# Optimization experiments

Hardware: AMD Instinct MI355X
Metric: run time of the kernel (lower is better)

The kernel has to match this reference:

```python
import jax, jax.numpy as jnp
import numpy as np

NH, NL, NPNT = 8, 4, 4          # heads, levels, points
NQ, BS, NK, D, DFFN = 100, 8, 18, 256, 1024
SPATIAL = np.array([[92, 92], [46, 46], [23, 23], [12, 12]], np.int32)
LEN_MEM = int((SPATIAL[:, 0] * SPATIAL[:, 1]).sum())  # 11253


def _layernorm(x, g, b):
    m = x.mean(-1, keepdims=True)
    v = ((x - m) ** 2).mean(-1, keepdims=True)
    return (x - m) / jnp.sqrt(v + 1e-5) * g + b


def _mha(xq, xk, xv, in_w, in_b, out_w, out_b):
    # torch nn.MultiheadAttention semantics, inputs (S, B, D)
    S, B, d = xq.shape
    dh = d // NH
    wq, wk, wv = jnp.split(in_w, 3, axis=0)
    bq, bk, bv = jnp.split(in_b, 3, axis=0)
    def proj(x, w, b):
        return (x @ w.T + b).reshape(x.shape[0], B, NH, dh).transpose(1, 2, 0, 3)
    q = proj(xq, wq, bq) * (1.0 / np.sqrt(dh))
    k = proj(xk, wk, bk)
    v = proj(xv, wv, bv)
    att = jax.nn.softmax(jnp.einsum('bhqd,bhkd->bhqk', q, k), axis=-1)
    o = jnp.einsum('bhqk,bhkd->bhqd', att, v).transpose(2, 0, 1, 3).reshape(S, B, d)
    return o @ out_w.T + out_b


def _bilinear(v_l, loc):
    # v_l: (bs,H,W,NH,dh); loc: (bs,Lq,NH,P,2) normalized [0,1]
    # matches F.grid_sample(align_corners=False, padding_mode='zeros')
    bs, H, W, nh, dh = v_l.shape
    x = loc[..., 0] * W - 0.5
    y = loc[..., 1] * H - 0.5
    x0 = jnp.floor(x); y0 = jnp.floor(y)
    lx = x - x0; ly = y - y0
    b_idx = jnp.arange(bs)[:, None, None, None]
    h_idx = jnp.arange(nh)[None, None, :, None]
    def corner(xa, ya, w):
        valid = (xa >= 0) & (xa < W) & (ya >= 0) & (ya < H)
        xi = jnp.clip(xa, 0, W - 1).astype(jnp.int32)
        yi = jnp.clip(ya, 0, H - 1).astype(jnp.int32)
        return v_l[b_idx, yi, xi, h_idx] * (w * valid)[..., None]
    return (corner(x0, y0, (1 - lx) * (1 - ly)) + corner(x0 + 1, y0, lx * (1 - ly))
            + corner(x0, y0 + 1, (1 - lx) * ly) + corner(x0 + 1, y0 + 1, lx * ly))


def _msda(q, rp, mem, pad_mask, ss, off_w, off_b, aw_w, aw_b, val_w, val_b, outp_w, outp_b):
    bs, Lq, d = q.shape
    dh = d // NH
    value = mem @ val_w.T + val_b
    value = jnp.where(pad_mask[..., None], 0.0, value).reshape(bs, -1, NH, dh)
    off = (q @ off_w.T + off_b).reshape(bs, Lq, NH, NL, NPNT, 2)
    aw = jax.nn.softmax((q @ aw_w.T + aw_b).reshape(bs, Lq, NH, NL * NPNT), -1)
    aw = aw.reshape(bs, Lq, NH, NL, NPNT)
    wh = jnp.asarray(ss[:, ::-1].copy(), jnp.float32)  # offset normalizer (W, H)
    loc = rp[:, :, None, :, None, :] + off / wh[None, None, None, :, None, :]
    out = jnp.zeros((bs, Lq, NH, dh), q.dtype)
    start = 0
    for l in range(NL):
        H, W = int(ss[l, 0]), int(ss[l, 1])
        v_l = value[:, start:start + H * W].reshape(bs, H, W, NH, dh)
        start += H * W
        samp = _bilinear(v_l, loc[:, :, :, l])          # (bs,Lq,NH,P,dh)
        out = out + (samp * aw[:, :, :, l, :, None]).sum(3)
    return out.reshape(bs, Lq, d) @ outp_w.T + outp_b


def _forward(tgt_pose, pos, ref_points, memory, w_in_w, w_in_b, w_out_w, w_out_b,
             a_in_w, a_in_b, a_out_w, a_out_b, off_w, off_b, aw_w, aw_b,
             val_w, val_b, outp_w, outp_b, wn_g, wn_b, an_g, an_b,
             n1_g, n1_b, n2_g, n2_b, l1_w, l1_b, l2_w, l2_b,
             spatial_shapes, level_start_index, padding_mask):
    ss = np.asarray(jax.device_get(spatial_shapes))
    nq, bs, nk, d = tgt_pose.shape
    # within-group self-attn over the nk keypoint tokens.
    # NOTE: with_pos_embed mutates tgt_pose in place in the torch code, so
    # q = k = v = tgt + pos and the residual also uses tgt + pos (faithful).
    t = tgt_pose + pos
    x = t.reshape(nq * bs, nk, d).transpose(1, 0, 2)   # (nk, nq*bs, d)
    a1 = _mha(x, x, x, w_in_w, w_in_b, w_out_w, w_out_b)
    t = _layernorm(t + a1.transpose(1, 0, 2).reshape(nq, bs, nk, d), wn_g, wn_b)
    # across-group self-attn over the nq groups
    x2 = t.reshape(nq, bs * nk, d)
    a2 = _mha(x2, x2, x2, a_in_w, a_in_b, a_out_w, a_out_b)
    t = _layernorm(t + a2.reshape(nq, bs, nk, d), an_g, an_b)
    # MSDeformAttn cross-attention (in-place pos add again, faithful)
    t = t + pos
    q = t.transpose(1, 0, 2, 3).reshape(bs, nq * nk, d)
    rp = jnp.swapaxes(ref_points, 0, 1)                # (bs, nq*nk, NL, 2)
    mem = jnp.swapaxes(memory, 0, 1)                   # (bs, LEN_MEM, d)
    c = _msda(q, rp, mem, padding_mask, ss, off_w, off_b, aw_w, aw_b,
              val_w, val_b, outp_w, outp_b)
    c = c.reshape(bs, nq, nk, d).transpose(1, 0, 2, 3)
    t = _layernorm(t + c, n1_g, n1_b)
    # FFN (dropout is identity in eval)
    h = jax.nn.relu(t @ l1_w.T + l1_b)
    return _layernorm(t + (h @ l2_w.T + l2_b), n2_g, n2_b)


def setup_inputs() -> dict:
    key = jax.random.key(0)
    ks = jax.random.split(key, 16)
    p = lambda k, shape: jax.random.normal(k, shape, jnp.float32) * 0.02
    lsi = np.concatenate([[0], np.cumsum(SPATIAL[:, 0] * SPATIAL[:, 1])[:-1]]).astype(np.int32)
    return {
        'tgt_pose': jax.random.normal(ks[0], (NQ, BS, NK, D), jnp.float32),
        'pos': jax.random.normal(ks[1], (NQ, BS, NK, D), jnp.float32),
        'ref_points': jax.random.uniform(ks[2], (NQ * NK, BS, NL, 2), jnp.float32),
        'memory': jax.random.normal(ks[3], (LEN_MEM, BS, D), jnp.float32),
        'w_in_w': p(ks[4], (3 * D, D)), 'w_in_b': jnp.zeros((3 * D,)),
        'w_out_w': p(ks[5], (D, D)), 'w_out_b': jnp.zeros((D,)),
        'a_in_w': p(ks[6], (3 * D, D)), 'a_in_b': jnp.zeros((3 * D,)),
        'a_out_w': p(ks[7], (D, D)), 'a_out_b': jnp.zeros((D,)),
        'off_w': p(ks[8], (NH * NL * NPNT * 2, D)),
        'off_b': jax.random.uniform(ks[9], (NH * NL * NPNT * 2,), jnp.float32, -2.0, 2.0),
        'aw_w': p(ks[10], (NH * NL * NPNT, D)), 'aw_b': jnp.zeros((NH * NL * NPNT,)),
        'val_w': p(ks[11], (D, D)), 'val_b': jnp.zeros((D,)),
        'outp_w': p(ks[12], (D, D)), 'outp_b': jnp.zeros((D,)),
        'wn_g': jnp.ones((D,)), 'wn_b': jnp.zeros((D,)),
        'an_g': jnp.ones((D,)), 'an_b': jnp.zeros((D,)),
        'n1_g': jnp.ones((D,)), 'n1_b': jnp.zeros((D,)),
        'n2_g': jnp.ones((D,)), 'n2_b': jnp.zeros((D,)),
        'l1_w': p(ks[13], (DFFN, D)), 'l1_b': jnp.zeros((DFFN,)),
        'l2_w': p(ks[14], (D, DFFN)), 'l2_b': jnp.zeros((D,)),
        'spatial_shapes': jnp.asarray(SPATIAL),
        'level_start_index': jnp.asarray(lsi),
        'padding_mask': jnp.zeros((BS, LEN_MEM), bool),
    }


def reference(tgt_pose, pos, ref_points, memory, w_in_w, w_in_b, w_out_w, w_out_b,
              a_in_w, a_in_b, a_out_w, a_out_b, off_w, off_b, aw_w, aw_b,
              val_w, val_b, outp_w, outp_b, wn_g, wn_b, an_g, an_b,
              n1_g, n1_b, n2_g, n2_b, l1_w, l1_b, l2_w, l2_b,
              spatial_shapes, level_start_index, padding_mask):
    return _forward(tgt_pose, pos, ref_points, memory, w_in_w, w_in_b, w_out_w, w_out_b,
                    a_in_w, a_in_b, a_out_w, a_out_b, off_w, off_b, aw_w, aw_b,
                    val_w, val_b, outp_w, outp_b, wn_g, wn_b, an_g, an_b,
                    n1_g, n1_b, n2_g, n2_b, l1_w, l1_b, l2_w, l2_b,
                    spatial_shapes, level_start_index, padding_mask)
```

## Files before the change

### kernel.cpp

```cpp
#include <hip/hip_runtime.h>
#include <math.h>

#define NH_ 8
#define D_ 256
#define NK_ 18
#define NQ_ 100
#define BS_ 8
#define LQ_ 1800
#define LEN_MEM_ 11253
#define NTOK_ 14400

typedef short bf16x8 __attribute__((ext_vector_type(8)));
typedef float f32x4 __attribute__((ext_vector_type(4)));
typedef unsigned short ushort;

__device__ inline ushort f2bf(float f) {
    unsigned int u = __builtin_bit_cast(unsigned int, f);
    unsigned int r = (u + 0x7fffu + ((u >> 16) & 1u)) >> 16;
    return (ushort)r;
}
__device__ inline float bf2f_hi(unsigned int u) {
    unsigned int i = u & 0xffff0000u;
    return __builtin_bit_cast(float, i);
}
__device__ inline float bf2f_lo(unsigned int u) {
    unsigned int i = u << 16;
    return __builtin_bit_cast(float, i);
}
__device__ inline int packbf2(float a, float b) {
    return (int)f2bf(a) | ((int)f2bf(b) << 16);
}

__global__ __launch_bounds__(256)
void wcvt_kernel(const float* s0, const float* s1, const float* s2, const float* s3,
                 const float* s4, const float* s5, const float* s6, const float* s7,
                 const float* s8, const float* s9, ushort* dst) {
    const int sizes[10] = {196608,65536,196608,65536,65536,32768,65536,65536,262144,262144};
    const int offs[10]  = {0,196608,262144,458752,524288,589824,622592,688128,753664,1015808};
    int ti = blockIdx.y;
    const float* s;
    switch (ti) {
        case 0: s = s0; break; case 1: s = s1; break; case 2: s = s2; break;
        case 3: s = s3; break; case 4: s = s4; break; case 5: s = s5; break;
        case 6: s = s6; break; case 7: s = s7; break; case 8: s = s8; break;
        default: s = s9; break;
    }
    int n = sizes[ti];
    int i = (blockIdx.x * 256 + threadIdx.x) * 8;
    if (i >= n) return;
    ushort* d = dst + offs[ti] + i;
    float4 f0 = *(const float4*)(s + i);
    float4 f1 = *(const float4*)(s + i + 4);
    int4 val;
    val.x = packbf2(f0.x, f0.y);
    val.y = packbf2(f0.z, f0.w);
    val.z = packbf2(f1.x, f1.y);
    val.w = packbf2(f1.z, f1.w);
    *(int4*)d = val;
}

__global__ __launch_bounds__(256)
void addcvt_kernel(const float* __restrict__ a, const float* __restrict__ b,
                   float* __restrict__ c, ushort* __restrict__ cbf, int n4) {
    int i = blockIdx.x * blockDim.x + threadIdx.x;
    if (i >= n4) return;
    float4 av = ((const float4*)a)[i];
    float4 bv = ((const float4*)b)[i];
    float4 cv;
    cv.x = av.x + bv.x; cv.y = av.y + bv.y; cv.z = av.z + bv.z; cv.w = av.w + bv.w;
    ((float4*)c)[i] = cv;
    uint2 p;
    p.x = (unsigned int)packbf2(cv.x, cv.y);
    p.y = (unsigned int)packbf2(cv.z, cv.w);
    *(uint2*)(cbf + (size_t)i * 4) = p;
}

template<int MODE, bool RELU, bool A_F32, bool OUT_BF16, int BN, int WAVES, int R>
__device__ __forceinline__
void gemmw_body(int bx, int by, const void* __restrict__ Av, const ushort* __restrict__ W,
                const float* __restrict__ bias, void* __restrict__ Cv,
                int M, int N, const unsigned char* __restrict__ mask, ushort* Ws) {
    constexpr int K = 256;
    constexpr int NT = BN / 16;
    const int tid = threadIdx.x;
    const int m0 = bx * (WAVES * 16 * R);
    const int n0 = by * BN;

    for (int c = tid; c < 32 * BN; c += WAVES * 64) {
        int kc = c & 31, n = c >> 5;
        int dst = kc * BN + (n ^ (kc & 7));
        *(int4*)(Ws + dst * 8) = *(const int4*)(W + (long)(n0 + n) * K + kc * 8);
    }
    __syncthreads();

    const int wv = tid >> 6, lane = tid & 63, fr = lane & 15, hi = lane >> 4;
    const int wm0 = m0 + wv * (16 * R);
    long arow[R];
#pragma unroll
    for (int r = 0; r < R; ++r) {
        int gr = wm0 + r * 16 + fr;
        if (gr > M - 1) gr = M - 1;
        if (MODE == 2) {
            int b = gr / LQ_; int lq = gr - b * LQ_;
            int q = lq / NK_; int kk = lq - q * NK_;
            arow[r] = (long)q * (BS_ * NK_) + b * NK_ + kk;
        } else {
            arow[r] = gr;
        }
    }

    f32x4 acc[R][NT];
#pragma unroll
    for (int r = 0; r < R; ++r)
#pragma unroll
        for (int t = 0; t < NT; ++t) acc[r][t] = f32x4{0.f, 0.f, 0.f, 0.f};

    if (A_F32) {
        const float* ap[R];
        float4 p0[R], p1[R];
#pragma unroll
        for (int r = 0; r < R; ++r) {
            ap[r] = (const float*)Av + arow[r] * (long)K + hi * 8;
            p0[r] = *(const float4*)ap[r];
            p1[r] = *(const float4*)(ap[r] + 4);
        }
#pragma unroll
        for (int ks = 0; ks < 8; ++ks) {
            bf16x8 cur[R];
#pragma unroll
            for (int r = 0; r < R; ++r) {
                int4 v;
                v.x = packbf2(p0[r].x, p0[r].y); v.y = packbf2(p0[r].z, p0[r].w);
                v.z = packbf2(p1[r].x, p1[r].y); v.w = packbf2(p1[r].z, p1[r].w);
                cur[r] = __builtin_bit_cast(bf16x8, v);
                if (ks < 7) {
                    p0[r] = *(const float4*)(ap[r] + (ks + 1) * 32);
                    p1[r] = *(const float4*)(ap[r] + (ks + 1) * 32 + 4);
                }
            }
            const int kc = ks * 4 + hi;
            const ushort* wb = Ws + ((kc * BN) + (fr ^ (kc & 7))) * 8;
#pragma unroll
            for (int t = 0; t < NT; ++t) {
                bf16x8 wf = *(const bf16x8*)(wb + t * 128);
#pragma unroll
                for (int r = 0; r < R; ++r)
                    acc[r][t] = __builtin_amdgcn_mfma_f32_16x16x32_bf16(cur[r], wf, acc[r][t], 0, 0, 0);
            }
        }
    } else {
        const ushort* ap[R];
        bf16x8 afrag[R];
#pragma unroll
        for (int r = 0; r < R; ++r) {
            ap[r] = (const ushort*)Av + arow[r] * (long)K + hi * 8;
            afrag[r] = *(const bf16x8*)ap[r];
        }
#pragma unroll
        for (int ks = 0; ks < 8; ++ks) {
            bf16x8 cur[R];
#pragma unroll
            for (int r = 0; r < R; ++r) {
                cur[r] = afrag[r];
                if (ks < 7) afrag[r] = *(const bf16x8*)(ap[r] + (ks + 1) * 32);
            }
            const int kc = ks * 4 + hi;
            const ushort* wb = Ws + ((kc * BN) + (fr ^ (kc & 7))) * 8;
#pragma unroll
            for (int t = 0; t < NT; ++t) {
                bf16x8 wf = *(const bf16x8*)(wb + t * 128);
#pragma unroll
                for (int r = 0; r < R; ++r)
                    acc[r][t] = __builtin_amdgcn_mfma_f32_16x16x32_bf16(cur[r], wf, acc[r][t], 0, 0, 0);
            }
        }
    }

#pragma unroll
    for (int r = 0; r < R; ++r) {
#pragma unroll
        for (int rr = 0; rr < 4; ++rr) {
            int gm = wm0 + r * 16 + hi * 4 + rr;
            if (gm >= M) continue;
            long orow = gm;
            bool zero = false;
            if (MODE == 1) {
                if (mask && mask[(size_t)(gm & 7) * LEN_MEM_ + (gm >> 3)]) zero = true;
            } else if (MODE == 3) {
                int b = gm / LQ_; int lq = gm - b * LQ_;
                int q = lq / NK_; int kk = lq - q * NK_;
                orow = (long)q * (BS_ * NK_) + b * NK_ + kk;
            }
#pragma unroll
            for (int t = 0; t < NT; ++t) {
                int gn = n0 + t * 16 + fr;
                float v = acc[r][t][rr] + bias[gn];
                if (RELU) v = fmaxf(v, 0.f);
                if (zero) v = 0.f;
                if (OUT_BF16) ((ushort*)Cv)[orow * (long)N + gn] = f2bf(v);
                else ((float*)Cv)[orow * (long)N + gn] = v;
            }
        }
    }
}

template<int MODE, bool RELU, bool A_F32, bool OUT_BF16, int BN, int WAVES, int R>
__global__ __launch_bounds__(WAVES * 64)
void gemmw_kernel(const void* __restrict__ Av, const ushort* __restrict__ W,
                  const float* __restrict__ bias, void* __restrict__ Cv,
                  int M, int N, const unsigned char* __restrict__ mask) {
    __shared__ ushort Ws[32 * BN * 8];
    gemmw_body<MODE, RELU, A_F32, OUT_BF16, BN, WAVES, R>(
        blockIdx.x, blockIdx.y, Av, W, bias, Cv, M, N, mask, Ws);
}

__global__ __launch_bounds__(512)
void fusedqv_kernel(const float* __restrict__ memA, const ushort* __restrict__ Wv,
                    const float* __restrict__ bv, ushort* __restrict__ Cval,
                    const unsigned char* __restrict__ mask, int voff,
                    const ushort* __restrict__ Aq, const ushort* __restrict__ Wq,
                    const float* __restrict__ bq, ushort* __restrict__ Cq) {
    __shared__ ushort Ws[32 * 128 * 8];
    int idx = blockIdx.x;
    if ((idx & 1) == 0) {
        int v = voff + (idx >> 1);
        gemmw_body<1, false, true, true, 128, 8, 2>(v >> 1, v & 1, memA, Wv, bv, Cval,
                                                    90024, 256, mask, Ws);
    } else {
        int q = idx >> 1;
        if (q < 342)
            gemmw_body<0, false, false, true, 128, 8, 2>(q % 57, q / 57, Aq, Wq, bq, Cq,
                                                         NTOK_, 768, nullptr, Ws);
    }
}

__global__ __launch_bounds__(256)
void fusedoa_kernel(const ushort* __restrict__ A,
                    const ushort* __restrict__ Woff, const float* __restrict__ boff, float* __restrict__ Coff,
                    const ushort* __restrict__ Waw, const float* __restrict__ baw, float* __restrict__ Caw) {
    __shared__ ushort Ws[32 * 64 * 8];
    int by = blockIdx.y;
    if (by < 4)
        gemmw_body<2, false, false, false, 64, 4, 2>(blockIdx.x, by, A, Woff, boff, Coff, NTOK_, 256, nullptr, Ws);
    else
        gemmw_body<2, false, false, false, 64, 4, 2>(blockIdx.x, by - 4, A, Waw, baw, Caw, NTOK_, 128, nullptr, Ws);
}

template<int MODE, bool RELU, bool A_F32, bool OUT_BF16>
__global__ __launch_bounds__(256)
void gemm_kernel(const void* __restrict__ Av, const ushort* __restrict__ W,
                 const float* __restrict__ bias, void* __restrict__ Cv,
                 int M, int N, int K, const unsigned char* __restrict__ mask) {
    constexpr int AST = 72;
    __shared__ ushort As[128 * AST];
    __shared__ ushort Bs[128 * AST];
    const int m0 = blockIdx.x * 128, n0 = blockIdx.y * 128;
    const int tid = threadIdx.x;
    const int w = tid >> 6, lane = tid & 63;
    const int wr = w >> 1, wc = w & 1;
    const int fr = lane & 15, hi = lane >> 4;
    f32x4 acc[4][4];
#pragma unroll
    for (int i = 0; i < 4; ++i)
#pragma unroll
        for (int j = 0; j < 4; ++j) acc[i][j] = f32x4{0.f, 0.f, 0.f, 0.f};

    const int srow = tid >> 1, shalf = tid & 1;
    long arow = 0;
    const bool avalid = (m0 + srow) < M;
    {
        int gr = m0 + srow;
        if (gr >= M) gr = M - 1;
        arow = gr;
    }

    for (int k0 = 0; k0 < K; k0 += 64) {
        ushort* ad = As + srow * AST + shalf * 32;
        if (avalid) {
            const ushort* ap = (const ushort*)Av + arow * (long)K + k0 + shalf * 32;
#pragma unroll
            for (int i = 0; i < 4; ++i) *(int4*)(ad + i * 8) = *(const int4*)(ap + i * 8);
        } else {
            int4 z = make_int4(0, 0, 0, 0);
#pragma unroll
            for (int i = 0; i < 4; ++i) *(int4*)(ad + i * 8) = z;
        }
        {
            const ushort* wp = W + (long)(n0 + srow) * K + k0 + shalf * 32;
            ushort* bd = Bs + srow * AST + shalf * 32;
#pragma unroll
            for (int i = 0; i < 4; ++i) *(int4*)(bd + i * 8) = *(const int4*)(wp + i * 8);
        }
        __syncthreads();
#pragma unroll
        for (int kb = 0; kb < 2; ++kb) {
            bf16x8 af[4], bfr[4];
#pragma unroll
            for (int i = 0; i < 4; ++i)
                af[i] = *(const bf16x8*)(As + (wr * 64 + i * 16 + fr) * AST + kb * 32 + hi * 8);
#pragma unroll
            for (int j = 0; j < 4; ++j)
                bfr[j] = *(const bf16x8*)(Bs + (wc * 64 + j * 16 + fr) * AST + kb * 32 + hi * 8);
#pragma unroll
            for (int i = 0; i < 4; ++i)
#pragma unroll
                for (int j = 0; j < 4; ++j)
                    acc[i][j] = __builtin_amdgcn_mfma_f32_16x16x32_bf16(af[i], bfr[j], acc[i][j], 0, 0, 0);
        }
        __syncthreads();
    }

#pragma unroll
    for (int i = 0; i < 4; ++i) {
#pragma unroll
        for (int r = 0; r < 4; ++r) {
            int gm = m0 + wr * 64 + i * 16 + hi * 4 + r;
            if (gm >= M) continue;
#pragma unroll
            for (int j = 0; j < 4; ++j) {
                int gn = n0 + wc * 64 + j * 16 + fr;
                float v = acc[i][j][r] + bias[gn];
                if (RELU) v = fmaxf(v, 0.f);
                if (OUT_BF16) ((ushort*)Cv)[(long)gm * N + gn] = f2bf(v);
                else ((float*)Cv)[(long)gm * N + gn] = v;
            }
        }
    }
}

template<int S, int SP, int HPB, int WAVES>
__global__ __launch_bounds__(WAVES * 64)
void mattn_kernel(const ushort* __restrict__ qkv, ushort* __restrict__ outb,
                  int rsG, int rsS) {
    constexpr int NTH = WAVES * 64;
    constexpr int SPk = ((SP + 31) / 32) * 32;
    constexpr int KST = 40;
    constexpr int PST = SPk + 8;
    constexpr int NT = SP / 16;
    constexpr int NB = HPB * NT;
    constexpr int HB = 8 / HPB;
    __shared__ ushort KsA[HPB * SP * KST];
    __shared__ ushort VtA[HPB * 32 * PST];
    __shared__ ushort PA [HPB * SP * PST];

    const int tid = threadIdx.x;
    const int g = blockIdx.x / HB;
    const int hbase = (blockIdx.x % HB) * HPB;

    for (int idx = tid; idx < HPB * S * 4; idx += NTH) {
        int hh = idx / (S * 4); int rem = idx - hh * (S * 4);
        int j = rem >> 2, q = rem & 3;
        const ushort* base = qkv + ((size_t)g * rsG + (size_t)j * rsS) * 768 + (hbase + hh) * 32 + q * 8;
        uint4 kv = *(const uint4*)(base + 256);
        ushort* kd = KsA + hh * (SP * KST) + j * KST + q * 8;
        *(uint2*)kd = make_uint2(kv.x, kv.y);
        *(uint2*)(kd + 4) = make_uint2(kv.z, kv.w);
        uint4 vv = *(const uint4*)(base + 512);
        ushort* vt = VtA + hh * (32 * PST) + j;
        unsigned int uu[4] = {vv.x, vv.y, vv.z, vv.w};
#pragma unroll
        for (int e = 0; e < 4; ++e) {
            vt[(q * 8 + e * 2    ) * PST] = (ushort)(uu[e] & 0xffff);
            vt[(q * 8 + e * 2 + 1) * PST] = (ushort)(uu[e] >> 16);
        }
    }
    for (int idx = tid; idx < HPB * 32 * (SPk - S); idx += NTH) {
        int hh = idx / (32 * (SPk - S)); int rem = idx - hh * (32 * (SPk - S));
        int d = rem / (SPk - S); int c = S + rem - d * (SPk - S);
        VtA[hh * 32 * PST + d * PST + c] = 0;
    }
    if constexpr (SPk > SP) {
        constexpr int PW = SPk - SP;
        for (int idx = tid; idx < HPB * SP * PW; idx += NTH) {
            int hh = idx / (SP * PW); int rem = idx - hh * (SP * PW);
            int rrow = rem / PW; int c = SP + rem - rrow * PW;
            PA[hh * SP * PST + rrow * PST + c] = 0;
        }
    }
    __syncthreads();

    const int wv = tid >> 6, lane = tid & 63, fr = lane & 15, hi = lane >> 4;
    for (int band = wv; band < NB; band += WAVES) {
        const int hh = band / NT, mb = band - (band / NT) * NT;
        const int h = hbase + hh;
        const ushort* Ks = KsA + hh * (SP * KST);
        const ushort* Vt = VtA + hh * (32 * PST);
        ushort* P = PA + hh * (SP * PST);

        int sq = mb * 16 + fr; if (sq > S - 1) sq = S - 1;
        bf16x8 qf = *(const bf16x8*)(qkv + ((size_t)g * rsG + (size_t)sq * rsS) * 768 + h * 32 + hi * 8);
        f32x4 sc[NT];
#pragma unroll
        for (int t = 0; t < NT; ++t) {
            bf16x8 kf = *(const bf16x8*)(Ks + (t * 16 + fr) * KST + hi * 8);
            sc[t] = __builtin_amdgcn_mfma_f32_16x16x32_bf16(qf, kf, f32x4{0.f, 0.f, 0.f, 0.f}, 0, 0, 0);
        }
#pragma unroll
        for (int t = 0; t < NT; ++t) {
            bool valid = (t * 16 + fr) < S;
#pragma unroll
            for (int r = 0; r < 4; ++r)
                sc[t][r] = valid ? sc[t][r] * 0.17677669529663687f : -1e30f;
        }
#pragma unroll
        for (int r = 0; r < 4; ++r) {
            float m = sc[0][r];
#pragma unroll
            for (int t = 1; t < NT; ++t) m = fmaxf(m, sc[t][r]);
            m = fmaxf(m, __shfl_xor(m, 1)); m = fmaxf(m, __shfl_xor(m, 2));
            m = fmaxf(m, __shfl_xor(m, 4)); m = fmaxf(m, __shfl_xor(m, 8));
            float e[NT]; float sum = 0.f;
#pragma unroll
            for (int t = 0; t < NT; ++t) { e[t] = __expf(sc[t][r] - m); sum += e[t]; }
            sum += __shfl_xor(sum, 1); sum += __shfl_xor(sum, 2);
            sum += __shfl_xor(sum, 4); sum += __shfl_xor(sum, 8);
            float inv = 1.f / sum;
            int row = mb * 16 + hi * 4 + r;
#pragma unroll
            for (int t = 0; t < NT; ++t)
                P[row * PST + t * 16 + fr] = f2bf(e[t] * inv);
        }
        f32x4 o0 = {0.f, 0.f, 0.f, 0.f}, o1 = {0.f, 0.f, 0.f, 0.f};
#pragma unroll
        for (int kb = 0; kb < SPk / 32; ++kb) {
            bf16x8 pf = *(const bf16x8*)(P + (mb * 16 + fr) * PST + kb * 32 + hi * 8);
            bf16x8 v0 = *(const bf16x8*)(Vt + fr * PST + kb * 32 + hi * 8);
            bf16x8 v1 = *(const bf16x8*)(Vt + (16 + fr) * PST + kb * 32 + hi * 8);
            o0 = __builtin_amdgcn_mfma_f32_16x16x32_bf16(pf, v0, o0, 0, 0, 0);
            o1 = __builtin_amdgcn_mfma_f32_16x16x32_bf16(pf, v1, o1, 0, 0, 0);
        }
#pragma unroll
        for (int r = 0; r < 4; ++r) {
            int s = mb * 16 + hi * 4 + r;
            if (s < S) {
                size_t ob = ((size_t)g * rsG + (size_t)s * rsS) * 256 + h * 32;
                outb[ob + fr] = f2bf(o0[r]);
                outb[ob + 16 + fr] = f2bf(o1[r]);
            }
        }
    }
}

__global__ __launch_bounds__(256)
void addln_kernel(const float* __restrict__ base, const ushort* __restrict__ delta,
                  const float* __restrict__ gamma, const float* __restrict__ beta,
                  const float* __restrict__ pos,
                  float* __restrict__ out, ushort* __restrict__ obf, int M) {
    int row = blockIdx.x * 4 + (threadIdx.x >> 6);
    int lane = threadIdx.x & 63;
    if (row >= M) return;
    const size_t rb = (size_t)row * 256 + lane * 4;
    float4 bv = *(const float4*)(base + rb);
    uint2 du = *(const uint2*)(delta + rb);
    float v[4];
    v[0] = bv.x + bf2f_lo(du.x);
    v[1] = bv.y + bf2f_hi(du.x);
    v[2] = bv.z + bf2f_lo(du.y);
    v[3] = bv.w + bf2f_hi(du.y);
    float s = v[0] + v[1] + v[2] + v[3];
#pragma unroll
    for (int off = 32; off; off >>= 1) s += __shfl_xor(s, off);
    float mean = s * (1.f / 256.f);
    float var = 0.f;
#pragma unroll
    for (int i = 0; i < 4; ++i) { float d = v[i] - mean; var += d * d; }
#pragma unroll
    for (int off = 32; off; off >>= 1) var += __shfl_xor(var, off);
    var *= (1.f / 256.f);
    float rstd = rsqrtf(var + 1e-5f);
    float4 gv = *(const float4*)(gamma + lane * 4);
    float4 bev = *(const float4*)(beta + lane * 4);
    float o[4];
    o[0] = (v[0] - mean) * rstd * gv.x + bev.x;
    o[1] = (v[1] - mean) * rstd * gv.y + bev.y;
    o[2] = (v[2] - mean) * rstd * gv.z + bev.z;
    o[3] = (v[3] - mean) * rstd * gv.w + bev.w;
    if (pos) {
        float4 pv = *(const float4*)(pos + rb);
        o[0] += pv.x; o[1] += pv.y; o[2] += pv.z; o[3] += pv.w;
    }
    float4 ov; ov.x = o[0]; ov.y = o[1]; ov.z = o[2]; ov.w = o[3];
    *(float4*)(out + rb) = ov;
    if (obf) {
        uint2 p;
        p.x = (unsigned int)packbf2(o[0], o[1]);
        p.y = (unsigned int)packbf2(o[2], o[3]);
        *(uint2*)(obf + rb) = p;
    }
}

__global__ __launch_bounds__(256)
void msda_kernel(const float* __restrict__ offb, const float* __restrict__ aw,
                 const ushort* __restrict__ val, const float* __restrict__ refp,
                 const int* __restrict__ spatial, const int* __restrict__ lsi,
                 ushort* __restrict__ samp) {
    const int unit = blockIdx.x * 32 + (threadIdx.x >> 3);
    const int lane8 = threadIdx.x & 7;
    const int base8 = (threadIdx.x & 63) & 56;
    const int h = unit & 7;
    const int t = unit >> 3;
    const int lq = t % LQ_;
    const int b = t / LQ_;
    const size_t row = (size_t)b * LQ_ + lq;

    float2 lg = *(const float2*)(aw + row * 128 + h * 16 + lane8 * 2);
    float m = fmaxf(lg.x, lg.y);
    m = fmaxf(m, __shfl_xor(m, 1)); m = fmaxf(m, __shfl_xor(m, 2)); m = fmaxf(m, __shfl_xor(m, 4));
    float e0 = __expf(lg.x - m), e1 = __expf(lg.y - m);
    float s = e0 + e1;
    s += __shfl_xor(s, 1); s += __shfl_xor(s, 2); s += __shfl_xor(s, 4);
    float inv = 1.f / s;
    float w0 = e0 * inv, w1 = e1 * inv;

    float4 of = *(const float4*)(offb + row * 256 + h * 32 + lane8 * 4);

    const float* rp = refp + ((size_t)lq * BS_ + b) * 8;
    float4 rp0 = *(const float4*)rp;
    float4 rp1 = *(const float4*)(rp + 4);

    float acc[4] = {0.f, 0.f, 0.f, 0.f};

#pragma unroll 1
    for (int lvl = 0; lvl < 4; ++lvl) {
        int H = spatial[lvl * 2], W = spatial[lvl * 2 + 1];
        int st = lsi[lvl];
        float rpx = (lvl == 0) ? rp0.x : (lvl == 1) ? rp0.z : (lvl == 2) ? rp1.x : rp1.z;
        float rpy = (lvl == 0) ? rp0.y : (lvl == 1) ? rp0.w : (lvl == 2) ? rp1.y : rp1.w;
        const ushort* vb = val + ((size_t)st * 8 + b) * 256 + h * 32 + lane8 * 4;
        float fW = (float)W, fH = (float)H;
#pragma unroll
        for (int p = 0; p < 4; ++p) {
            float ox_ = (p & 1) ? of.z : of.x;
            float oy_ = (p & 1) ? of.w : of.y;
            float wp_ = (p & 1) ? w1 : w0;
            int src = base8 + lvl * 2 + (p >> 1);
            float ox  = __shfl(ox_, src);
            float oy  = __shfl(oy_, src);
            float wpt = __shfl(wp_, src);

            float x = rpx * fW + ox - 0.5f;
            float y = rpy * fH + oy - 0.5f;
            float x0f = floorf(x), y0f = floorf(y);
            float lx = x - x0f, ly = y - y0f;
            int x0 = (int)x0f, y0 = (int)y0f;
            int xc0 = min(max(x0, 0), W - 1), xc1 = min(max(x0 + 1, 0), W - 1);
            int yc0 = min(max(y0, 0), H - 1), yc1 = min(max(y0 + 1, 0), H - 1);
            float vx0 = (x0 >= 0 && x0 < W) ? 1.f : 0.f;
            float vx1 = (x0 >= -1 && x0 + 1 < W) ? 1.f : 0.f;
            float vy0 = (y0 >= 0 && y0 < H) ? 1.f : 0.f;
            float vy1 = (y0 >= -1 && y0 + 1 < H) ? 1.f : 0.f;
            float w00 = wpt * (1.f - lx) * (1.f - ly) * vx0 * vy0;
            float w10 = wpt * lx * (1.f - ly) * vx1 * vy0;
            float w01 = wpt * (1.f - lx) * ly * vx0 * vy1;
            float w11 = wpt * lx * ly * vx1 * vy1;
            uint2 u00 = *(const uint2*)(vb + (size_t)(yc0 * W + xc0) * 2048);
            uint2 u10 = *(const uint2*)(vb + (size_t)(yc0 * W + xc1) * 2048);
            uint2 u01 = *(const uint2*)(vb + (size_t)(yc1 * W + xc0) * 2048);
            uint2 u11 = *(const uint2*)(vb + (size_t)(yc1 * W + xc1) * 2048);
            acc[0] += w00 * bf2f_lo(u00.x) + w10 * bf2f_lo(u10.x)
                    + w01 * bf2f_lo(u01.x) + w11 * bf2f_lo(u11.x);
            acc[1] += w00 * bf2f_hi(u00.x) + w10 * bf2f_hi(u10.x)
                    + w01 * bf2f_hi(u01.x) + w11 * bf2f_hi(u11.x);
            acc[2] += w00 * bf2f_lo(u00.y) + w10 * bf2f_lo(u10.y)
                    + w01 * bf2f_lo(u01.y) + w11 * bf2f_lo(u11.y);
            acc[3] += w00 * bf2f_hi(u00.y) + w10 * bf2f_hi(u10.y)
                    + w01 * bf2f_hi(u01.y) + w11 * bf2f_hi(u11.y);
        }
    }
    size_t o = row * 256 + h * 32 + lane8 * 4;
    uint2 pk;
    pk.x = (unsigned int)packbf2(acc[0], acc[1]);
    pk.y = (unsigned int)packbf2(acc[2], acc[3]);
    *(uint2*)(samp + o) = pk;
}

extern "C" void kernel_launch(void* const* d_in, const int* in_sizes, int n_in,
                              void* d_out, int out_size, void* d_ws, size_t ws_size,
                              hipStream_t stream) {
    const float* tgt     = (const float*)d_in[0];
    const float* pos     = (const float*)d_in[1];
    const float* refp    = (const float*)d_in[2];
    const float* memory  = (const float*)d_in[3];
    const float* w_in_w  = (const float*)d_in[4];
    const float* w_in_b  = (const float*)d_in[5];
    const float* w_out_w = (const float*)d_in[6];
    const float* w_out_b = (const float*)d_in[7];
    const float* a_in_w  = (const float*)d_in[8];
    const float* a_in_b  = (const float*)d_in[9];
    const float* a_out_w = (const float*)d_in[10];
    const float* a_out_b = (const float*)d_in[11];
    const float* off_w   = (const float*)d_in[12];
    const float* off_b   = (const float*)d_in[13];
    const float* aw_w    = (const float*)d_in[14];
    const float* aw_b    = (const float*)d_in[15];
    const float* val_w   = (const float*)d_in[16];
    const float* val_b   = (const float*)d_in[17];
    const float* outp_w  = (const float*)d_in[18];
    const float* outp_b  = (const float*)d_in[19];
    const float* wn_g    = (const float*)d_in[20];
    const float* wn_b    = (const float*)d_in[21];
    const float* an_g    = (const float*)d_in[22];
    const float* an_b    = (const float*)d_in[23];
    const float* n1_g    = (const float*)d_in[24];
    const float* n1_b    = (const float*)d_in[25];
    const float* n2_g    = (const float*)d_in[26];
    const float* n2_b    = (const float*)d_in[27];
    const float* l1_w    = (const float*)d_in[28];
    const float* l1_b    = (const float*)d_in[29];
    const float* l2_w    = (const float*)d_in[30];
    const float* l2_b    = (const float*)d_in[31];
    const int*   spatial = (const int*)d_in[32];
    const int*   lsi     = (const int*)d_in[33];
    const unsigned char* pmask = (const unsigned char*)d_in[34];
    float* out = (float*)d_out;

    float*  T      = (float*)d_ws;
    ushort* Tbf    = (ushort*)(T + 3686400);
    ushort* B16    = Tbf + 3686400;
    ushort* CBbf   = B16 + 11059200;
    ushort* VALbf  = CBbf + 3686400;
    ushort* SAMPbf = VALbf + 23046144;
    ushort* Hbf    = SAMPbf + 3686400;
    ushort* WB     = Hbf + 14745600;
    float*  OFF    = (float*)(WB + 1277952);
    float*  AW     = OFF + 3686400;
    ushort* OFFbf  = (ushort*)(AW + 1843200);

    ushort* WB_win  = WB + 0;
    ushort* WB_wout = WB + 196608;
    ushort* WB_ain  = WB + 262144;
    ushort* WB_aout = WB + 458752;
    ushort* WB_off  = WB + 524288;
    ushort* WB_aw   = WB + 589824;
    ushort* WB_val  = WB + 622592;
    ushort* WB_outp = WB + 688128;
    ushort* WB_l1   = WB + 753664;
    ushort* WB_l2   = WB + 1015808;

    const int n4 = NTOK_ * 256 / 4;

    wcvt_kernel<<<dim3(128, 10), 256, 0, stream>>>(
        w_in_w, w_out_w, a_in_w, a_out_w, off_w, aw_w, val_w, outp_w, l1_w, l2_w, WB);
    addcvt_kernel<<<n4 / 256, 256, 0, stream>>>(tgt, pos, T, Tbf, n4);
    fusedqv_kernel<<<704, 512, 0, stream>>>(
        memory, WB_val, val_b, VALbf, pmask, 0, Tbf, WB_win, w_in_b, B16);
    mattn_kernel<18, 32, 4, 4><<<800 * 2, 256, 0, stream>>>(B16, CBbf, 18, 1);
    gemmw_kernel<0, false, false, true, 64, 4, 2><<<dim3(113, 4), 256, 0, stream>>>(
        CBbf, WB_wout, w_out_b, OFFbf, NTOK_, 256, nullptr);
    addln_kernel<<<NTOK_ / 4, 256, 0, stream>>>(T, OFFbf, wn_g, wn_b, nullptr, T, Tbf, NTOK_);
    fusedqv_kernel<<<704, 512, 0, stream>>>(
        memory, WB_val, val_b, VALbf, pmask, 352, Tbf, WB_ain, a_in_b, B16);
    mattn_kernel<100, 112, 1, 7><<<144 * 8, 448, 0, stream>>>(B16, CBbf, 1, 144);
    gemmw_kernel<0, false, false, true, 64, 4, 2><<<dim3(113, 4), 256, 0, stream>>>(
        CBbf, WB_aout, a_out_b, OFFbf, NTOK_, 256, nullptr);
    addln_kernel<<<NTOK_ / 4, 256, 0, stream>>>(T, OFFbf, an_g, an_b, pos, T, Tbf, NTOK_);
    fusedoa_kernel<<<dim3(113, 6), 256, 0, stream>>>(
        Tbf, WB_off, off_b, OFF, WB_aw, aw_b, AW);
    msda_kernel<<<3600, 256, 0, stream>>>(OFF, AW, VALbf, refp, spatial, lsi, SAMPbf);
    gemmw_kernel<3, false, false, true, 64, 4, 2><<<dim3(113, 4), 256, 0, stream>>>(
        SAMPbf, WB_outp, outp_b, OFFbf, NTOK_, 256, nullptr);
    addln_kernel<<<NTOK_ / 4, 256, 0, stream>>>(T, OFFbf, n1_g, n1_b, nullptr, T, Tbf, NTOK_);
    gemmw_kernel<0, true, false, true, 64, 4, 2><<<dim3(113, 16), 256, 0, stream>>>(
        Tbf, WB_l1, l1_b, Hbf, NTOK_, 1024, nullptr);
    gemm_kernel<0, false, false, true><<<dim3(113, 2), 256, 0, stream>>>(
        Hbf, WB_l2, l2_b, OFFbf, NTOK_, 256, 1024, nullptr);
    addln_kernel<<<NTOK_ / 4, 256, 0, stream>>>(T, OFFbf, n2_g, n2_b, nullptr, out, nullptr, NTOK_);
}
```

Before: 324.2 us.

## Split FFN down-projection along K and move value projection into one fused launch

The FFN down-projection GEMM (K=1024) now splits K into two halves across blockIdx.z, writing two bf16 partial outputs that the final add+layernorm kernel sums. This doubles the block count from 226 to 452 to fill more CUs. The value-projection blocks that were spread over two fused launches now run entirely in the first fused launch, interleaved 2:1 with the self-attention QKV blocks. The cross-attention in-projection becomes a standalone GEMM. The cost is an extra bf16 partial-sum round trip and bf16 rounding of each partial before the sum.

```diff
diff --git a/kernel.cpp b/kernel.cpp
--- a/kernel.cpp
+++ b/kernel.cpp
@@ -217,17 +217,18 @@
 __global__ __launch_bounds__(512)
 void fusedqv_kernel(const float* __restrict__ memA, const ushort* __restrict__ Wv,
                     const float* __restrict__ bv, ushort* __restrict__ Cval,
-                    const unsigned char* __restrict__ mask, int voff,
+                    const unsigned char* __restrict__ mask,
                     const ushort* __restrict__ Aq, const ushort* __restrict__ Wq,
                     const float* __restrict__ bq, ushort* __restrict__ Cq) {
     __shared__ ushort Ws[32 * 128 * 8];
     int idx = blockIdx.x;
-    if ((idx & 1) == 0) {
-        int v = voff + (idx >> 1);
+    int g3 = idx / 3, r3 = idx - g3 * 3;
+    if (r3 < 2) {
+        int v = g3 * 2 + r3;
         gemmw_body<1, false, true, true, 128, 8, 2>(v >> 1, v & 1, memA, Wv, bv, Cval,
                                                     90024, 256, mask, Ws);
     } else {
-        int q = idx >> 1;
+        int q = g3;
         if (q < 342)
             gemmw_body<0, false, false, true, 128, 8, 2>(q % 57, q / 57, Aq, Wq, bq, Cq,
                                                          NTOK_, 768, nullptr, Ws);
@@ -246,15 +247,17 @@
         gemmw_body<2, false, false, false, 64, 4, 2>(blockIdx.x, by - 4, A, Waw, baw, Caw, NTOK_, 128, nullptr, Ws);
 }
 
-template<int MODE, bool RELU, bool A_F32, bool OUT_BF16>
 __global__ __launch_bounds__(256)
-void gemm_kernel(const void* __restrict__ Av, const ushort* __restrict__ W,
-                 const float* __restrict__ bias, void* __restrict__ Cv,
-                 int M, int N, int K, const unsigned char* __restrict__ mask) {
+void ffndown_kernel(const ushort* __restrict__ Av, const ushort* __restrict__ W,
+                    const float* __restrict__ bias, ushort* __restrict__ C0,
+                    ushort* __restrict__ C1, int M, int N) {
     constexpr int AST = 72;
+    constexpr int LD = 1024;
     __shared__ ushort As[128 * AST];
     __shared__ ushort Bs[128 * AST];
     const int m0 = blockIdx.x * 128, n0 = blockIdx.y * 128;
+    const int kz = blockIdx.z * 512;
+    ushort* C = blockIdx.z ? C1 : C0;
     const int tid = threadIdx.x;
     const int w = tid >> 6, lane = tid & 63;
     const int wr = w >> 1, wc = w & 1;
@@ -266,7 +269,7 @@
         for (int j = 0; j < 4; ++j) acc[i][j] = f32x4{0.f, 0.f, 0.f, 0.f};
 
     const int srow = tid >> 1, shalf = tid & 1;
-    long arow = 0;
+    long arow;
     const bool avalid = (m0 + srow) < M;
     {
         int gr = m0 + srow;
@@ -274,10 +277,10 @@
         arow = gr;
     }
 
-    for (int k0 = 0; k0 < K; k0 += 64) {
+    for (int k0 = 0; k0 < 512; k0 += 64) {
         ushort* ad = As + srow * AST + shalf * 32;
         if (avalid) {
-            const ushort* ap = (const ushort*)Av + arow * (long)K + k0 + shalf * 32;
+            const ushort* ap = Av + arow * (long)LD + kz + k0 + shalf * 32;
 #pragma unroll
             for (int i = 0; i < 4; ++i) *(int4*)(ad + i * 8) = *(const int4*)(ap + i * 8);
         } else {
@@ -286,7 +289,7 @@
             for (int i = 0; i < 4; ++i) *(int4*)(ad + i * 8) = z;
         }
         {
-            const ushort* wp = W + (long)(n0 + srow) * K + k0 + shalf * 32;
+            const ushort* wp = W + (long)(n0 + srow) * LD + kz + k0 + shalf * 32;
             ushort* bd = Bs + srow * AST + shalf * 32;
 #pragma unroll
             for (int i = 0; i < 4; ++i) *(int4*)(bd + i * 8) = *(const int4*)(wp + i * 8);
@@ -319,10 +322,8 @@
 #pragma unroll
             for (int j = 0; j < 4; ++j) {
                 int gn = n0 + wc * 64 + j * 16 + fr;
-                float v = acc[i][j][r] + bias[gn];
-                if (RELU) v = fmaxf(v, 0.f);
-                if (OUT_BF16) ((ushort*)Cv)[(long)gm * N + gn] = f2bf(v);
-                else ((float*)Cv)[(long)gm * N + gn] = v;
+                float v = acc[i][j][r] + (blockIdx.z ? 0.f : bias[gn]);
+                C[(long)gm * N + gn] = f2bf(v);
             }
         }
     }
@@ -443,6 +444,7 @@
 
 __global__ __launch_bounds__(256)
 void addln_kernel(const float* __restrict__ base, const ushort* __restrict__ delta,
+                  const ushort* __restrict__ delta2,
                   const float* __restrict__ gamma, const float* __restrict__ beta,
                   const float* __restrict__ pos,
                   float* __restrict__ out, ushort* __restrict__ obf, int M) {
@@ -457,6 +459,11 @@
     v[1] = bv.y + bf2f_hi(du.x);
     v[2] = bv.z + bf2f_lo(du.y);
     v[3] = bv.w + bf2f_hi(du.y);
+    if (delta2) {
+        uint2 d2 = *(const uint2*)(delta2 + rb);
+        v[0] += bf2f_lo(d2.x); v[1] += bf2f_hi(d2.x);
+        v[2] += bf2f_lo(d2.y); v[3] += bf2f_hi(d2.y);
+    }
     float s = v[0] + v[1] + v[2] + v[3];
 #pragma unroll
     for (int off = 32; off; off >>= 1) s += __shfl_xor(s, off);
@@ -625,6 +632,7 @@
     float*  OFF    = (float*)(WB + 1277952);
     float*  AW     = OFF + 3686400;
     ushort* OFFbf  = (ushort*)(AW + 1843200);
+    ushort* OFF2bf = OFFbf + 3686400;
 
     ushort* WB_win  = WB + 0;
     ushort* WB_wout = WB + 196608;
@@ -642,27 +650,27 @@
     wcvt_kernel<<<dim3(128, 10), 256, 0, stream>>>(
         w_in_w, w_out_w, a_in_w, a_out_w, off_w, aw_w, val_w, outp_w, l1_w, l2_w, WB);
     addcvt_kernel<<<n4 / 256, 256, 0, stream>>>(tgt, pos, T, Tbf, n4);
-    fusedqv_kernel<<<704, 512, 0, stream>>>(
-        memory, WB_val, val_b, VALbf, pmask, 0, Tbf, WB_win, w_in_b, B16);
+    fusedqv_kernel<<<3 * 352, 512, 0, stream>>>(
+        memory, WB_val, val_b, VALbf, pmask, Tbf, WB_win, w_in_b, B16);
     mattn_kernel<18, 32, 4, 4><<<800 * 2, 256, 0, stream>>>(B16, CBbf, 18, 1);
     gemmw_kernel<0, false, false, true, 64, 4, 2><<<dim3(113, 4), 256, 0, stream>>>(
         CBbf, WB_wout, w_out_b, OFFbf, NTOK_, 256, nullptr);
-    addln_kernel<<<NTOK_ / 4, 256, 0, stream>>>(T, OFFbf, wn_g, wn_b, nullptr, T, Tbf, NTOK_);
-    fusedqv_kernel<<<704, 512, 0, stream>>>(
-        memory, WB_val, val_b, VALbf, pmask, 352, Tbf, WB_ain, a_in_b, B16);
+    addln_kernel<<<NTOK_ / 4, 256, 0, stream>>>(T, OFFbf, nullptr, wn_g, wn_b, nullptr, T, Tbf, NTOK_);
+    gemmw_kernel<0, false, false, true, 64, 4, 2><<<dim3(113, 12), 256, 0, stream>>>(
+        Tbf, WB_ain, a_in_b, B16, NTOK_, 768, nullptr);
     mattn_kernel<100, 112, 1, 7><<<144 * 8, 448, 0, stream>>>(B16, CBbf, 1, 144);
     gemmw_kernel<0, false, false, true, 64, 4, 2><<<dim3(113, 4), 256, 0, stream>>>(
         CBbf, WB_aout, a_out_b, OFFbf, NTOK_, 256, nullptr);
-    addln_kernel<<<NTOK_ / 4, 256, 0, stream>>>(T, OFFbf, an_g, an_b, pos, T, Tbf, NTOK_);
+    addln_kernel<<<NTOK_ / 4, 256, 0, stream>>>(T, OFFbf, nullptr, an_g, an_b, pos, T, Tbf, NTOK_);
     fusedoa_kernel<<<dim3(113, 6), 256, 0, stream>>>(
         Tbf, WB_off, off_b, OFF, WB_aw, aw_b, AW);
     msda_kernel<<<3600, 256, 0, stream>>>(OFF, AW, VALbf, refp, spatial, lsi, SAMPbf);
     gemmw_kernel<3, false, false, true, 64, 4, 2><<<dim3(113, 4), 256, 0, stream>>>(
         SAMPbf, WB_outp, outp_b, OFFbf, NTOK_, 256, nullptr);
-    addln_kernel<<<NTOK_ / 4, 256, 0, stream>>>(T, OFFbf, n1_g, n1_b, nullptr, T, Tbf, NTOK_);
+    addln_kernel<<<NTOK_ / 4, 256, 0, stream>>>(T, OFFbf, nullptr, n1_g, n1_b, nullptr, T, Tbf, NTOK_);
     gemmw_kernel<0, true, false, true, 64, 4, 2><<<dim3(113, 16), 256, 0, stream>>>(
         Tbf, WB_l1, l1_b, Hbf, NTOK_, 1024, nullptr);
-    gemm_kernel<0, false, false, true><<<dim3(113, 2), 256, 0, stream>>>(
-        Hbf, WB_l2, l2_b, OFFbf, NTOK_, 256, 1024, nullptr);
-    addln_kernel<<<NTOK_ / 4, 256, 0, stream>>>(T, OFFbf, n2_g, n2_b, nullptr, out, nullptr, NTOK_);
-}
+    ffndown_kernel<<<dim3(113, 2, 2), 256, 0, stream>>>(
+        Hbf, WB_l2, l2_b, OFFbf, OFF2bf, NTOK_, 256);
+    addln_kernel<<<NTOK_ / 4, 256, 0, stream>>>(T, OFFbf, OFF2bf, n2_g, n2_b, nullptr, out, nullptr, NTOK_);
+}
```

Measured after the change: 316.9 us. 2.3% less time.
